# Kernel tuning notes

Hardware: AMD Instinct MI355X
Metric: run time of the kernel (lower is better)

Reference implementation:

```python
import math
import jax, jax.numpy as jnp
import numpy as np

N, MA, DESIGN, RADIAL, SOFTENING, RM = 8, 24, 26, 15, 3, 5.0


def setup_inputs() -> dict:
    key = jax.random.key(0)
    k1, k2 = jax.random.split(key, 2)
    # atomic coordinates, spread out so interatomic distances are realistic (bohr)
    coords = jax.random.normal(k1, (N, MA, 3), jnp.float32) * 3.0
    # labels all >= 0 -> full padding (padding[i] == MA for every molecule)
    labels = jax.random.randint(k2, (N, MA), 0, 10)
    # deterministic synthetic Lebedev-like design (26 points on the unit sphere)
    phi = jnp.linspace(0.0, 2.0 * math.pi, DESIGN, endpoint=False).astype(jnp.float32)
    psi = jnp.linspace(0.1, math.pi - 0.1, DESIGN).astype(jnp.float32)
    sphere = jnp.stack([jnp.cos(phi) * jnp.sin(psi),
                        jnp.sin(phi) * jnp.sin(psi),
                        jnp.cos(psi)], axis=1)           # [D, 3]
    sphere_weights = jnp.full((DESIGN,), 1.0 / DESIGN, dtype=jnp.float32)
    return {"labels": labels, "coords": coords,
            "sphere": sphere, "sphere_weights": sphere_weights}


def _spheric_grid(sphere, sphere_weights):
    # Gauss-Chebyshev radial quadrature mapped by the Becke transform
    i = jnp.arange(1, RADIAL + 1, dtype=jnp.float32)
    z = -jnp.cos(math.pi * (2.0 * i - 1.0) / (2.0 * RADIAL))
    dr = 2.0 * RM * (1.0 - z) ** -2
    r = RM * (1.0 + z) / (1.0 - z)
    w = jnp.sqrt(1.0 - z ** 2) * dr * math.pi / RADIAL
    w = r ** 2 * 4.0 * math.pi * w                       # [R]
    conc = (r[:, None, None] * sphere[None]).reshape(-1, 3)          # [R*D, 3]
    wt = (sphere_weights[None, :] * w[:, None]).reshape(-1)          # [R*D]
    return conc, wt


def _becke(x, r, dm, idx):
    # x [n, mx, 3] grid points, r [n, M, 3] centers, dm [n, M, M], idx [mx]
    rx = jnp.linalg.norm(x[:, :, None, :] - r[:, None, :, :], axis=-1)   # [n, mx, M]
    # elliptic coordinate mu_ij for every grid point: [n, mx, M, M]
    mu = (rx[..., :, None] - rx[..., None, :]) / jnp.clip(dm[:, None], 1e-12, None)
    for _ in range(1, SOFTENING):                       # softening passes
        mu = 0.5 * mu * (3.0 - mu ** 2)
    mu = 0.5 * (1.0 - mu)
    mu = mu + 0.5 * jnp.eye(dm.shape[-1], dtype=x.dtype)  # diagonal -> 1
    cell = jnp.prod(mu, axis=-1)                        # [n, mx, M] cell functions
    v_i = jnp.take_along_axis(cell, idx[None, :, None], axis=2)[..., 0]
    return v_i / cell.sum(axis=2)


def reference(labels, coords, sphere, sphere_weights):
    # labels are all >= 0 here, so padding == MA for every molecule and the
    # original per-molecule loop collapses into one batched computation.
    conc, wt = _spheric_grid(sphere, sphere_weights)    # conc [ms,3], wt [ms]
    ms = conc.shape[0]
    n, M, _ = coords.shape
    dm = jnp.linalg.norm(coords[:, :, None, :] - coords[:, None, :, :], axis=-1)
    # place concentric spheres on each atom (atom-major ordering, as in torch)
    grid = (coords[:, :, None, :] + conc[None, None]).reshape(n, M * ms, 3)
    w_full = jnp.broadcast_to(wt[None, :], (M, ms)).reshape(-1)      # [M*ms]
    idx = jnp.repeat(jnp.arange(M), ms)                              # sample -> center
    v = _becke(grid, coords, dm, idx)                                # [n, M*ms]
    weights = v * w_full[None, :]
    dv = grid[:, :, None, :] - coords[:, None, :, :]                 # [n, M*ms, M, 3]
    return grid, dv, weights
```

## Files before the change

### kernel.cpp

```cpp
#include <hip/hip_runtime.h>
#include <math.h>

constexpr int MAC = 24;
constexpr int DES = 26;
constexpr int RAD = 15;
constexpr int MS  = RAD * DES;
constexpr int MX  = MAC * MS;
constexpr int NCHUNK = (MX + 255) / 256;

__global__ __launch_bounds__(256) void becke_grid_kernel(
    const float* __restrict__ coords,
    const float* __restrict__ sphere,
    const float* __restrict__ sw,
    float* __restrict__ out_grid,
    float* __restrict__ out_dv,
    float* __restrict__ out_w)
{
    __shared__ float cs[MAC * 3];
    __shared__ float inv_dm[MAC][MAC];
    __shared__ float sph[DES * 3];
    __shared__ float sws[DES];
    __shared__ float rr[RAD];
    __shared__ float ww[RAD];
    __shared__ float rxs[256][MAC + 1];

    const int tid   = threadIdx.x;
    const int n     = blockIdx.x / NCHUNK;
    const int chunk = blockIdx.x - n * NCHUNK;

    for (int e = tid; e < MAC * 3; e += 256) cs[e] = coords[n * MAC * 3 + e];
    for (int e = tid; e < DES * 3; e += 256) sph[e] = sphere[e];
    if (tid < DES) sws[tid] = sw[tid];
    if (tid < RAD) {
        double i   = (double)tid + 1.0;
        double z   = -cos(M_PI * (2.0 * i - 1.0) / (2.0 * (double)RAD));
        double omz = 1.0 - z;
        double dr  = 2.0 * 5.0 / (omz * omz);
        double r   = 5.0 * (1.0 + z) / omz;
        double w1  = sqrt(1.0 - z * z) * dr * M_PI / (double)RAD;
        double w   = r * r * 4.0 * M_PI * w1;
        rr[tid] = (float)r;
        ww[tid] = (float)w;
    }
    __syncthreads();
    for (int e = tid; e < MAC * MAC; e += 256) {
        int i = e / MAC, j = e - (e / MAC) * MAC;
        float dx = cs[i * 3 + 0] - cs[j * 3 + 0];
        float dy = cs[i * 3 + 1] - cs[j * 3 + 1];
        float dz = cs[i * 3 + 2] - cs[j * 3 + 2];
        float dd = sqrtf(dx * dx + dy * dy + dz * dz);
        inv_dm[i][j] = 1.0f / fmaxf(dd, 1e-12f);
    }
    __syncthreads();

    const int s = chunk * 256 + tid;
    if (s >= MX) return;

    const int a = s / MS;
    const int t = s - a * MS;
    const int k = t / DES;
    const int d = t - k * DES;

    const float r  = rr[k];
    const float gx = cs[a * 3 + 0] + r * sph[d * 3 + 0];
    const float gy = cs[a * 3 + 1] + r * sph[d * 3 + 1];
    const float gz = cs[a * 3 + 2] + r * sph[d * 3 + 2];

    {
        size_t gb = ((size_t)n * MX + s) * 3;
        out_grid[gb + 0] = gx;
        out_grid[gb + 1] = gy;
        out_grid[gb + 2] = gz;
    }

    const size_t dvb = ((size_t)n * MX + s) * (MAC * 3);
    #pragma unroll
    for (int j = 0; j < MAC; ++j) {
        float dx = gx - cs[j * 3 + 0];
        float dy = gy - cs[j * 3 + 1];
        float dz = gz - cs[j * 3 + 2];
        out_dv[dvb + j * 3 + 0] = dx;
        out_dv[dvb + j * 3 + 1] = dy;
        out_dv[dvb + j * 3 + 2] = dz;
        rxs[tid][j] = sqrtf(dx * dx + dy * dy + dz * dz);
    }

    float cell_sum = 0.0f, cell_a = 0.0f;
    for (int i = 0; i < MAC; ++i) {
        const float rxi = rxs[tid][i];
        float p = 1.0f;
        #pragma unroll
        for (int j = 0; j < MAC; ++j) {
            float mu = (rxi - rxs[tid][j]) * inv_dm[i][j];
            mu = 0.5f * mu * (3.0f - mu * mu);
            mu = 0.5f * mu * (3.0f - mu * mu);
            float sij = 0.5f * (1.0f - mu);
            p *= (i == j) ? 1.0f : sij;
        }
        cell_sum += p;
        if (i == a) cell_a = p;
    }

    const float v = cell_a / cell_sum;
    out_w[(size_t)n * MX + s] = v * sws[d] * ww[k];
}

extern "C" void kernel_launch(void* const* d_in, const int* in_sizes, int n_in,
                              void* d_out, int out_size, void* d_ws, size_t ws_size,
                              hipStream_t stream) {
    const float* coords = (const float*)d_in[1];
    const float* sphere = (const float*)d_in[2];
    const float* sw     = (const float*)d_in[3];

    const int nmol = in_sizes[1] / (MAC * 3);

    float* o    = (float*)d_out;
    float* ogrid = o;
    float* odv   = ogrid + (size_t)nmol * MX * 3;
    float* ow    = odv + (size_t)nmol * MX * MAC * 3;

    becke_grid_kernel<<<dim3(nmol * NCHUNK), dim3(256), 0, stream>>>(
        coords, sphere, sw, ogrid, odv, ow);
}
```

Baseline: 92.55 us.

## Assign one thread per (grid point, atom) pair and reduce cell functions in shared memory

Work is redistributed so that each block handles 16 grid points with 24 threads per point, one per atom. Each thread computes one dv triple and one cell-function product, which cuts per-thread serial work 24-fold and makes the dv stores contiguous across neighbouring threads. A final shared-memory reduction by 16 threads forms the normalized weight. The cost is more blocks, an extra barrier per block, and repeated setup of the shared tables (inv_dm and constants) for every 16 points.

```diff
diff --git a/kernel.cpp b/kernel.cpp
--- a/kernel.cpp
+++ b/kernel.cpp
@@ -6,9 +6,11 @@
 constexpr int RAD = 15;
 constexpr int MS  = RAD * DES;
 constexpr int MX  = MAC * MS;
-constexpr int NCHUNK = (MX + 255) / 256;
+constexpr int PTS = 16;
+constexpr int BTH = PTS * MAC;
+constexpr int BPM = MX / PTS;
 
-__global__ __launch_bounds__(256) void becke_grid_kernel(
+__global__ __launch_bounds__(BTH) void becke_kernel(
     const float* __restrict__ coords,
     const float* __restrict__ sphere,
     const float* __restrict__ sw,
@@ -17,92 +19,104 @@
     float* __restrict__ out_w)
 {
     __shared__ float cs[MAC * 3];
-    __shared__ float inv_dm[MAC][MAC];
+    __shared__ float inv_dm[MAC][MAC + 1];
     __shared__ float sph[DES * 3];
     __shared__ float sws[DES];
     __shared__ float rr[RAD];
     __shared__ float ww[RAD];
-    __shared__ float rxs[256][MAC + 1];
+    __shared__ float rxs[PTS][MAC];
+    __shared__ float cell[PTS][MAC];
 
-    const int tid   = threadIdx.x;
-    const int n     = blockIdx.x / NCHUNK;
-    const int chunk = blockIdx.x - n * NCHUNK;
+    const int tid = threadIdx.x;
+    const int n   = blockIdx.x / BPM;
+    const int s0  = (blockIdx.x - n * BPM) * PTS;
 
-    for (int e = tid; e < MAC * 3; e += 256) cs[e] = coords[n * MAC * 3 + e];
-    for (int e = tid; e < DES * 3; e += 256) sph[e] = sphere[e];
-    if (tid < DES) sws[tid] = sw[tid];
-    if (tid < RAD) {
-        double i   = (double)tid + 1.0;
+    if (tid < MAC * 3) cs[tid] = coords[n * MAC * 3 + tid];
+    if (tid >= 128 && tid < 128 + DES * 3) sph[tid - 128] = sphere[tid - 128];
+    if (tid >= 224 && tid < 224 + DES) sws[tid - 224] = sw[tid - 224];
+    if (tid >= 256 && tid < 256 + RAD) {
+        double i   = (double)(tid - 256) + 1.0;
         double z   = -cos(M_PI * (2.0 * i - 1.0) / (2.0 * (double)RAD));
         double omz = 1.0 - z;
         double dr  = 2.0 * 5.0 / (omz * omz);
-        double r   = 5.0 * (1.0 + z) / omz;
+        double rq  = 5.0 * (1.0 + z) / omz;
         double w1  = sqrt(1.0 - z * z) * dr * M_PI / (double)RAD;
-        double w   = r * r * 4.0 * M_PI * w1;
-        rr[tid] = (float)r;
-        ww[tid] = (float)w;
-    }
-    __syncthreads();
-    for (int e = tid; e < MAC * MAC; e += 256) {
-        int i = e / MAC, j = e - (e / MAC) * MAC;
-        float dx = cs[i * 3 + 0] - cs[j * 3 + 0];
-        float dy = cs[i * 3 + 1] - cs[j * 3 + 1];
-        float dz = cs[i * 3 + 2] - cs[j * 3 + 2];
-        float dd = sqrtf(dx * dx + dy * dy + dz * dz);
-        inv_dm[i][j] = 1.0f / fmaxf(dd, 1e-12f);
+        rr[tid - 256] = (float)rq;
+        ww[tid - 256] = (float)(rq * rq * 4.0 * M_PI * w1);
     }
     __syncthreads();
 
-    const int s = chunk * 256 + tid;
-    if (s >= MX) return;
+    for (int e = tid; e < MAC * MAC; e += BTH) {
+        int ii = e / MAC, jj = e - ii * MAC;
+        float dx = cs[ii * 3 + 0] - cs[jj * 3 + 0];
+        float dy = cs[ii * 3 + 1] - cs[jj * 3 + 1];
+        float dz = cs[ii * 3 + 2] - cs[jj * 3 + 2];
+        float dd = sqrtf(dx * dx + dy * dy + dz * dz);
+        inv_dm[ii][jj] = 1.0f / fmaxf(dd, 1e-12f);
+    }
 
+    const int p = tid / MAC;
+    const int i = tid - p * MAC;
+    const int s = s0 + p;
     const int a = s / MS;
     const int t = s - a * MS;
     const int k = t / DES;
     const int d = t - k * DES;
 
-    const float r  = rr[k];
-    const float gx = cs[a * 3 + 0] + r * sph[d * 3 + 0];
-    const float gy = cs[a * 3 + 1] + r * sph[d * 3 + 1];
-    const float gz = cs[a * 3 + 2] + r * sph[d * 3 + 2];
+    const float rq = rr[k];
+    const float gx = cs[a * 3 + 0] + rq * sph[d * 3 + 0];
+    const float gy = cs[a * 3 + 1] + rq * sph[d * 3 + 1];
+    const float gz = cs[a * 3 + 2] + rq * sph[d * 3 + 2];
 
-    {
+    if (i == 0) {
         size_t gb = ((size_t)n * MX + s) * 3;
         out_grid[gb + 0] = gx;
         out_grid[gb + 1] = gy;
         out_grid[gb + 2] = gz;
     }
 
-    const size_t dvb = ((size_t)n * MX + s) * (MAC * 3);
+    const float dx = gx - cs[i * 3 + 0];
+    const float dy = gy - cs[i * 3 + 1];
+    const float dz = gz - cs[i * 3 + 2];
+    {
+        size_t dvb = (((size_t)n * MX + s) * MAC + i) * 3;
+        out_dv[dvb + 0] = dx;
+        out_dv[dvb + 1] = dy;
+        out_dv[dvb + 2] = dz;
+    }
+    const float rxi = sqrtf(dx * dx + dy * dy + dz * dz);
+    rxs[p][i] = rxi;
+    __syncthreads();
+
+    float rxl[MAC];
+    #pragma unroll
+    for (int j = 0; j < MAC; ++j) rxl[j] = rxs[p][j];
+
+    float prod = 1.0f;
     #pragma unroll
     for (int j = 0; j < MAC; ++j) {
-        float dx = gx - cs[j * 3 + 0];
-        float dy = gy - cs[j * 3 + 1];
-        float dz = gz - cs[j * 3 + 2];
-        out_dv[dvb + j * 3 + 0] = dx;
-        out_dv[dvb + j * 3 + 1] = dy;
-        out_dv[dvb + j * 3 + 2] = dz;
-        rxs[tid][j] = sqrtf(dx * dx + dy * dy + dz * dz);
+        float mu = (rxi - rxl[j]) * inv_dm[i][j];
+        mu = 0.5f * mu * (3.0f - mu * mu);
+        mu = 0.5f * mu * (3.0f - mu * mu);
+        float sij = 0.5f * (1.0f - mu);
+        prod *= (j == i) ? 1.0f : sij;
     }
+    cell[p][i] = prod;
+    __syncthreads();
 
-    float cell_sum = 0.0f, cell_a = 0.0f;
-    for (int i = 0; i < MAC; ++i) {
-        const float rxi = rxs[tid][i];
-        float p = 1.0f;
+    if (tid < PTS) {
+        const int pp = tid;
+        const int ss = s0 + pp;
+        const int aa = ss / MS;
+        const int tt = ss - aa * MS;
+        const int kk = tt / DES;
+        const int dd = tt - kk * DES;
+        float sum = 0.0f;
         #pragma unroll
-        for (int j = 0; j < MAC; ++j) {
-            float mu = (rxi - rxs[tid][j]) * inv_dm[i][j];
-            mu = 0.5f * mu * (3.0f - mu * mu);
-            mu = 0.5f * mu * (3.0f - mu * mu);
-            float sij = 0.5f * (1.0f - mu);
-            p *= (i == j) ? 1.0f : sij;
-        }
-        cell_sum += p;
-        if (i == a) cell_a = p;
+        for (int j = 0; j < MAC; ++j) sum += cell[pp][j];
+        const float v = cell[pp][aa] / sum;
+        out_w[(size_t)n * MX + ss] = v * sws[dd] * ww[kk];
     }
-
-    const float v = cell_a / cell_sum;
-    out_w[(size_t)n * MX + s] = v * sws[d] * ww[k];
 }
 
 extern "C" void kernel_launch(void* const* d_in, const int* in_sizes, int n_in,
@@ -114,11 +128,11 @@
 
     const int nmol = in_sizes[1] / (MAC * 3);
 
-    float* o    = (float*)d_out;
+    float* o     = (float*)d_out;
     float* ogrid = o;
     float* odv   = ogrid + (size_t)nmol * MX * 3;
     float* ow    = odv + (size_t)nmol * MX * MAC * 3;
 
-    becke_grid_kernel<<<dim3(nmol * NCHUNK), dim3(256), 0, stream>>>(
+    becke_kernel<<<dim3(nmol * BPM), dim3(BTH), 0, stream>>>(
         coords, sphere, sw, ogrid, odv, ow);
 }
```

New measurement: 86.26 us. -6.8%, faster.

## Map one grid point per 32-lane group with shuffle-based Becke cell products

Applied to the files above, without the earlier changes.

Splits the work into a tiny precompute kernel (inverse interatomic distances, shell offsets, weights) and a main kernel where each grid point is handled by 32 lanes, one lane per atom. Each lane computes one cell-function product using shuffles of the distances and a row of inverse distances held in registers, then the lanes reduce with xor-shuffles. The goal is to remove the serial 24x24 loop per thread and the large shared-memory scratch, and to make the dv writes more coalesced. The cost is a second launch, 8 idle lanes out of every 32, and a dependency on workspace memory.

```diff
diff --git a/kernel.cpp b/kernel.cpp
--- a/kernel.cpp
+++ b/kernel.cpp
@@ -6,103 +6,114 @@
 constexpr int RAD = 15;
 constexpr int MS  = RAD * DES;
 constexpr int MX  = MAC * MS;
-constexpr int NCHUNK = (MX + 255) / 256;
+constexpr int PPB = 8;
+constexpr int BPM = MX / PPB;
 
-__global__ __launch_bounds__(256) void becke_grid_kernel(
-    const float* __restrict__ coords,
-    const float* __restrict__ sphere,
-    const float* __restrict__ sw,
-    float* __restrict__ out_grid,
-    float* __restrict__ out_dv,
-    float* __restrict__ out_w)
+__global__ __launch_bounds__(512) void becke_precompute(
+    const float* __restrict__ coords, const float* __restrict__ sphere,
+    const float* __restrict__ sw, int nmol,
+    float* __restrict__ inv_dm, float* __restrict__ conc4, float* __restrict__ wt)
 {
-    __shared__ float cs[MAC * 3];
-    __shared__ float inv_dm[MAC][MAC];
-    __shared__ float sph[DES * 3];
-    __shared__ float sws[DES];
-    __shared__ float rr[RAD];
-    __shared__ float ww[RAD];
-    __shared__ float rxs[256][MAC + 1];
-
-    const int tid   = threadIdx.x;
-    const int n     = blockIdx.x / NCHUNK;
-    const int chunk = blockIdx.x - n * NCHUNK;
-
-    for (int e = tid; e < MAC * 3; e += 256) cs[e] = coords[n * MAC * 3 + e];
-    for (int e = tid; e < DES * 3; e += 256) sph[e] = sphere[e];
-    if (tid < DES) sws[tid] = sw[tid];
+    __shared__ float rr[RAD], ww[RAD];
+    const int tid = threadIdx.x;
     if (tid < RAD) {
         double i   = (double)tid + 1.0;
         double z   = -cos(M_PI * (2.0 * i - 1.0) / (2.0 * (double)RAD));
         double omz = 1.0 - z;
-        double dr  = 2.0 * 5.0 / (omz * omz);
+        double dr  = 10.0 / (omz * omz);
         double r   = 5.0 * (1.0 + z) / omz;
         double w1  = sqrt(1.0 - z * z) * dr * M_PI / (double)RAD;
-        double w   = r * r * 4.0 * M_PI * w1;
         rr[tid] = (float)r;
-        ww[tid] = (float)w;
+        ww[tid] = (float)(r * r * 4.0 * M_PI * w1);
     }
     __syncthreads();
-    for (int e = tid; e < MAC * MAC; e += 256) {
-        int i = e / MAC, j = e - (e / MAC) * MAC;
-        float dx = cs[i * 3 + 0] - cs[j * 3 + 0];
-        float dy = cs[i * 3 + 1] - cs[j * 3 + 1];
-        float dz = cs[i * 3 + 2] - cs[j * 3 + 2];
+    for (int t = tid; t < MS; t += 512) {
+        int k = t / DES, d = t - k * DES;
+        conc4[t * 4 + 0] = rr[k] * sphere[d * 3 + 0];
+        conc4[t * 4 + 1] = rr[k] * sphere[d * 3 + 1];
+        conc4[t * 4 + 2] = rr[k] * sphere[d * 3 + 2];
+        conc4[t * 4 + 3] = 0.0f;
+        wt[t] = sw[d] * ww[k];
+    }
+    for (int e = tid; e < nmol * MAC * MAC; e += 512) {
+        int n = e / (MAC * MAC), r0 = e - n * MAC * MAC;
+        int i = r0 / MAC, j = r0 - i * MAC;
+        const float* cb = coords + n * MAC * 3;
+        float dx = cb[i * 3 + 0] - cb[j * 3 + 0];
+        float dy = cb[i * 3 + 1] - cb[j * 3 + 1];
+        float dz = cb[i * 3 + 2] - cb[j * 3 + 2];
         float dd = sqrtf(dx * dx + dy * dy + dz * dz);
-        inv_dm[i][j] = 1.0f / fmaxf(dd, 1e-12f);
+        inv_dm[e] = 1.0f / fmaxf(dd, 1e-12f);
     }
-    __syncthreads();
+}
 
-    const int s = chunk * 256 + tid;
-    if (s >= MX) return;
+__global__ __launch_bounds__(256) void becke_main(
+    const float* __restrict__ coords,
+    const float* __restrict__ inv_dm,
+    const float* __restrict__ conc4,
+    const float* __restrict__ wt,
+    float* __restrict__ og,
+    float* __restrict__ odv,
+    float* __restrict__ ow)
+{
+    const int tid = threadIdx.x;
+    const int l   = tid & 31;
+    const int n   = blockIdx.x / BPM;
+    const int sm  = (blockIdx.x - n * BPM) * PPB + (tid >> 5);
+    const int a   = sm / MS;
+    const int t   = sm - a * MS;
+    const bool act = (l < MAC);
+    const int  i   = act ? l : (MAC - 1);
 
-    const int a = s / MS;
-    const int t = s - a * MS;
-    const int k = t / DES;
-    const int d = t - k * DES;
+    const float4 cc  = *reinterpret_cast<const float4*>(conc4 + t * 4);
+    const float  wtt = wt[t];
+    const float* cb  = coords + n * MAC * 3;
 
-    const float r  = rr[k];
-    const float gx = cs[a * 3 + 0] + r * sph[d * 3 + 0];
-    const float gy = cs[a * 3 + 1] + r * sph[d * 3 + 1];
-    const float gz = cs[a * 3 + 2] + r * sph[d * 3 + 2];
+    const float gx = cb[a * 3 + 0] + cc.x;
+    const float gy = cb[a * 3 + 1] + cc.y;
+    const float gz = cb[a * 3 + 2] + cc.z;
 
-    {
-        size_t gb = ((size_t)n * MX + s) * 3;
-        out_grid[gb + 0] = gx;
-        out_grid[gb + 1] = gy;
-        out_grid[gb + 2] = gz;
+    const float dx = gx - cb[i * 3 + 0];
+    const float dy = gy - cb[i * 3 + 1];
+    const float dz = gz - cb[i * 3 + 2];
+    const size_t sg = (size_t)n * MX + sm;
+    if (act) {
+        float* dvp = odv + (sg * MAC + i) * 3;
+        dvp[0] = dx; dvp[1] = dy; dvp[2] = dz;
+    }
+    const float rxi = sqrtf(dx * dx + dy * dy + dz * dz);
+
+    float inv[MAC];
+    const float* irow = inv_dm + (n * MAC + i) * MAC;
+    #pragma unroll
+    for (int q = 0; q < MAC / 4; ++q) {
+        float4 v = *reinterpret_cast<const float4*>(irow + q * 4);
+        inv[q * 4 + 0] = v.x; inv[q * 4 + 1] = v.y;
+        inv[q * 4 + 2] = v.z; inv[q * 4 + 3] = v.w;
     }
 
-    const size_t dvb = ((size_t)n * MX + s) * (MAC * 3);
+    float prod = 1.0f;
     #pragma unroll
     for (int j = 0; j < MAC; ++j) {
-        float dx = gx - cs[j * 3 + 0];
-        float dy = gy - cs[j * 3 + 1];
-        float dz = gz - cs[j * 3 + 2];
-        out_dv[dvb + j * 3 + 0] = dx;
-        out_dv[dvb + j * 3 + 1] = dy;
-        out_dv[dvb + j * 3 + 2] = dz;
-        rxs[tid][j] = sqrtf(dx * dx + dy * dy + dz * dz);
+        float rxj = __shfl(rxi, j, 32);
+        float mu  = (rxi - rxj) * inv[j];
+        mu *= fmaf(mu * mu, -0.5f, 1.5f);
+        mu *= fmaf(mu * mu, -0.5f, 1.5f);
+        prod *= fmaf(mu, -0.5f, 0.5f);
     }
+    float cell = act ? (prod + prod) : 0.0f;
 
-    float cell_sum = 0.0f, cell_a = 0.0f;
-    for (int i = 0; i < MAC; ++i) {
-        const float rxi = rxs[tid][i];
-        float p = 1.0f;
-        #pragma unroll
-        for (int j = 0; j < MAC; ++j) {
-            float mu = (rxi - rxs[tid][j]) * inv_dm[i][j];
-            mu = 0.5f * mu * (3.0f - mu * mu);
-            mu = 0.5f * mu * (3.0f - mu * mu);
-            float sij = 0.5f * (1.0f - mu);
-            p *= (i == j) ? 1.0f : sij;
-        }
-        cell_sum += p;
-        if (i == a) cell_a = p;
+    float sum = cell;
+    #pragma unroll
+    for (int m = 16; m >= 1; m >>= 1) sum += __shfl_xor(sum, m, 32);
+    const float ca = __shfl(cell, a, 32);
+
+    if (l == MAC) {
+        float* gp = og + sg * 3;
+        gp[0] = gx; gp[1] = gy; gp[2] = gz;
+    } else if (l == MAC + 1) {
+        ow[sg] = (ca / sum) * wtt;
     }
-
-    const float v = cell_a / cell_sum;
-    out_w[(size_t)n * MX + s] = v * sws[d] * ww[k];
 }
 
 extern "C" void kernel_launch(void* const* d_in, const int* in_sizes, int n_in,
@@ -114,11 +125,18 @@
 
     const int nmol = in_sizes[1] / (MAC * 3);
 
-    float* o    = (float*)d_out;
+    float* ws     = (float*)d_ws;
+    float* inv_dm = ws;
+    float* conc4  = inv_dm + (size_t)nmol * MAC * MAC;
+    float* wtab   = conc4 + MS * 4;
+
+    float* o     = (float*)d_out;
     float* ogrid = o;
     float* odv   = ogrid + (size_t)nmol * MX * 3;
-    float* ow    = odv + (size_t)nmol * MX * MAC * 3;
+    float* owt   = odv + (size_t)nmol * MX * MAC * 3;
 
-    becke_grid_kernel<<<dim3(nmol * NCHUNK), dim3(256), 0, stream>>>(
-        coords, sphere, sw, ogrid, odv, ow);
+    becke_precompute<<<dim3(1), dim3(512), 0, stream>>>(
+        coords, sphere, sw, nmol, inv_dm, conc4, wtab);
+    becke_main<<<dim3(nmol * BPM), dim3(256), 0, stream>>>(
+        coords, inv_dm, conc4, wtab, ogrid, odv, owt);
 }
```

Measured after the change: 84.06 us. 1.1x faster.
